# Performance work log

Measured on AMD Instinct MI355X. Metric: run time of the kernel, lower is better.

Reference implementation:

```python
import jax, jax.numpy as jnp
import numpy as np

DEPTH = 8
INPUT_DIM = 256
OUTPUT_DIM = 32
BATCH = 131072
N_INNER = 2 ** DEPTH - 1   # 255 inner nodes in heap/level order
N_LEAF = 2 ** DEPTH        # 256 leaves


def setup_inputs() -> dict:
    key = jax.random.key(0)
    kx, kw, kb, kbeta, kleaf = jax.random.split(key, 5)
    x = jax.random.normal(kx, (BATCH, INPUT_DIM), dtype=jnp.float32)
    # Stacked per-node Linear(input_dim, 1): weight rows [N_INNER, INPUT_DIM], bias [N_INNER]
    W = jax.random.normal(kw, (N_INNER, INPUT_DIM), dtype=jnp.float32) / np.sqrt(INPUT_DIM)
    b = jax.random.normal(kb, (N_INNER,), dtype=jnp.float32) * 0.01
    beta = jax.random.normal(kbeta, (N_INNER,), dtype=jnp.float32)  # per-node beta scalar
    leaf_param = jax.random.normal(kleaf, (N_LEAF, OUTPUT_DIM), dtype=jnp.float32)
    return {"x": x, "W": W, "b": b, "beta": beta, "leaf_param": leaf_param}


def _soft_tree(x, W, b, beta, leaf_param):
    B = x.shape[0]
    # All inner-node splits in one GEMM: sigmoid(beta_n * (x @ w_n + b_n))
    prob = jax.nn.sigmoid(beta[None, :] * (x @ W.T + b[None, :]))  # [B, N_INNER]
    # Level-wise path probability propagation (nodes stored in heap/level order).
    p = jnp.ones((B, 1), dtype=x.dtype)
    for d in range(DEPTH):
        lo = 2 ** d - 1
        pr = prob[:, lo: lo + 2 ** d]                      # [B, 2^d]
        # left child gets p*pr, right child gets p*(1-pr); interleave to keep DFS order
        p = jnp.stack([p * pr, p * (1.0 - pr)], axis=-1).reshape(B, 2 ** (d + 1))
    # leaf distributions Q = softmax(param) broadcast over batch; mixture output
    Q = jax.nn.softmax(leaf_param, axis=-1)                # [N_LEAF, OUTPUT_DIM]
    out = p @ Q                                            # [B, OUTPUT_DIM]
    return out, p


def reference(x, W, b, beta, leaf_param):
    out, path_probs = _soft_tree(x, W, b, beta, leaf_param)
    return out, path_probs
```

## Files before the change

### kernel.cpp

```cpp
#include <hip/hip_runtime.h>

#define BATCH   131072
#define IN_DIM  256
#define OUT_DIM 32
#define N_INNER 255
#define N_LEAF  256
#define OUT_HDR (BATCH * OUT_DIM)

#define TILE_M  64
#define BK      32
#define NTHR    512
#define NCHUNK  8
#define PSTR    260
#define INV64K  (1.0f / 65536.0f)

#define WS_QT_HI   0
#define WS_QT_LO   16384
#define WS_WIMG_HI 32768
#define WS_WIMG_LO (32768 + 131072)

#define WB0 0
#define WB1 32768
#define XB0 65536
#define XB1 73728
#define IMG_LO 34816
#define SMEM_BYTES 81920

typedef __attribute__((ext_vector_type(8))) short bf16x8;
typedef __attribute__((ext_vector_type(4))) float f32x4;

__device__ __forceinline__ unsigned short bf16rne(float a) {
    unsigned u = __float_as_uint(a);
    return (unsigned short)((u + 0x7FFFu + ((u >> 16) & 1u)) >> 16);
}
__device__ __forceinline__ unsigned packhi2(float a, float b) {
    return (unsigned)bf16rne(a) | ((unsigned)bf16rne(b) << 16);
}
__device__ __forceinline__ unsigned packlo2(float a, float b) {
    unsigned short ha = bf16rne(a), hb = bf16rne(b);
    float ra = a - __uint_as_float((unsigned)ha << 16);
    float rb = b - __uint_as_float((unsigned)hb << 16);
    return (unsigned)bf16rne(ra) | ((unsigned)bf16rne(rb) << 16);
}
__device__ __forceinline__ void split2(float a, float b, unsigned& hi, unsigned& lo) {
    unsigned short ha = bf16rne(a), hb = bf16rne(b);
    hi = (unsigned)ha | ((unsigned)hb << 16);
    float ra = a - __uint_as_float((unsigned)ha << 16);
    float rb = b - __uint_as_float((unsigned)hb << 16);
    lo = (unsigned)bf16rne(ra) | ((unsigned)bf16rne(rb) << 16);
}
__device__ __forceinline__ void tsplit2(float a, float b, unsigned& h, unsigned& l) {
    unsigned ua = __float_as_uint(a), ub = __float_as_uint(b);
    h = (ua >> 16) | (ub & 0xFFFF0000u);
    float ra = a - __uint_as_float(ua & 0xFFFF0000u);
    float rb = b - __uint_as_float(ub & 0xFFFF0000u);
    l = (__float_as_uint(ra) >> 16) | (__float_as_uint(rb) & 0xFFFF0000u);
}

__device__ __forceinline__ void gload16(const void* g, void* l) {
    __builtin_amdgcn_global_load_lds(
        (const __attribute__((address_space(1))) unsigned int*)g,
        (__attribute__((address_space(3))) unsigned int*)l, 16, 0, 0);
}

__global__ void wsplit_k(const float* __restrict__ W,
                         unsigned int* __restrict__ whi, unsigned int* __restrict__ wlo) {
    int gid = blockIdx.x * 512 + threadIdx.x;
    int n   = gid >> 5;
    int oct = gid & 31;
    float4 a = make_float4(0.f,0.f,0.f,0.f), b = a;
    if (n < N_INNER) {
        a = *(const float4*)(W + (size_t)n * IN_DIM + oct * 8);
        b = *(const float4*)(W + (size_t)n * IN_DIM + oct * 8 + 4);
    }
    uint4 h, l;
    split2(a.x, a.y, h.x, l.x); split2(a.z, a.w, h.y, l.y);
    split2(b.x, b.y, h.z, l.z); split2(b.z, b.w, h.w, l.w);
    int c = oct >> 2, kg = oct & 3;
    size_t off = ((size_t)(c * 4 + kg) * 256 + n) * 4;
    *(uint4*)(whi + off) = h;
    *(uint4*)(wlo + off) = l;
}

__global__ void qt_k(const float* __restrict__ leaf,
                     unsigned short* __restrict__ qhi, unsigned short* __restrict__ qlo) {
    int l = threadIdx.x;
    const float* row = leaf + l * OUT_DIM;
    float v[OUT_DIM];
    float mx = -1e30f;
#pragma unroll
    for (int o = 0; o < OUT_DIM; ++o) { v[o] = row[o]; mx = fmaxf(mx, v[o]); }
    float s = 0.f;
#pragma unroll
    for (int o = 0; o < OUT_DIM; ++o) { v[o] = __expf(v[o] - mx); s += v[o]; }
    float r = 1.f / s;
#pragma unroll
    for (int o = 0; o < OUT_DIM; ++o) {
        float q = v[o] * r;
        unsigned short h = bf16rne(q);
        float res = q - __uint_as_float((unsigned)h << 16);
        qhi[o * 256 + l] = h;
        qlo[o * 256 + l] = bf16rne(res);
    }
}

#define TREE_STAGE(D) { \
    const int base_ = (1 << (D)) - 1 + (qq << ((D) - 3)); \
    _Pragma("unroll") \
    for (int i = (1 << ((D) - 3)) - 1; i >= 0; --i) { \
        float pr_ = (float)pb[base_ + i] * INV64K; \
        float a_  = P[i]; \
        float lv_ = a_ * pr_; \
        P[2*i]     = lv_; \
        P[2*i + 1] = a_ - lv_; \
    } }

#define MFMA_BF16(A, B, C) __builtin_amdgcn_mfma_f32_16x16x32_bf16(A, B, C, 0, 0, 0)

__launch_bounds__(NTHR, 4)
__global__ void tree_k(const float* __restrict__ x,
                       const float* __restrict__ bv, const float* __restrict__ beta,
                       const unsigned short* __restrict__ qhi, const unsigned short* __restrict__ qlo,
                       const char* __restrict__ wimg_hi, const char* __restrict__ wimg_lo,
                       float* __restrict__ out) {
    extern __shared__ char smem[];
    const int tid  = threadIdx.x;
    const int row0 = blockIdx.x * TILE_M;

    const int lane  = tid & 63;
    const int w     = tid >> 6;
    const int col16 = lane & 15;
    const int hi4   = lane >> 4;
    const int wr    = w >> 2;
    const int wc    = w & 3;

    f32x4 acc[2][4];
#pragma unroll
    for (int i = 0; i < 2; ++i)
#pragma unroll
        for (int j = 0; j < 4; ++j) acc[i][j] = (f32x4){0.f, 0.f, 0.f, 0.f};

    const int xrow = tid >> 3;
    const int xkq  = tid & 7;
    const int xoff = (xkq >> 1) * 1024 + xrow * 16 + (xkq & 1) * 8;
    const float* xsrc = x + (size_t)(row0 + xrow) * IN_DIM + xkq * 4;

    {
        char* dh = smem + WB0 + w * 1024;
        char* dl = dh + 16384;
        gload16(wimg_hi + tid * 16,        dh);
        gload16(wimg_hi + 8192 + tid * 16, dh + 8192);
        gload16(wimg_lo + tid * 16,        dl);
        gload16(wimg_lo + 8192 + tid * 16, dl + 8192);
        float4 v = *(const float4*)(xsrc);
        uint2 h, l;
        tsplit2(v.x, v.y, h.x, l.x);
        tsplit2(v.z, v.w, h.y, l.y);
        *(uint2*)(smem + XB0 + xoff)        = h;
        *(uint2*)(smem + XB0 + 4096 + xoff) = l;
    }
    __syncthreads();

#pragma unroll 1
    for (int c = 0; c < NCHUNK; ++c) {
        const int cur = c & 1;
        const char* wb = smem + (cur ? WB1 : WB0);
        const char* xb = smem + (cur ? XB1 : XB0);
        char* wbn = smem + (cur ? WB0 : WB1);
        char* xbn = smem + (cur ? XB0 : XB1);

        float4 xn;
        const bool more = (c + 1 < NCHUNK);
        if (more) {
            const char* gh = wimg_hi + (size_t)(c + 1) * 16384;
            const char* gl = wimg_lo + (size_t)(c + 1) * 16384;
            char* dh = wbn + w * 1024;
            char* dl = dh + 16384;
            gload16(gh + tid * 16,        dh);
            gload16(gh + 8192 + tid * 16, dh + 8192);
            gload16(gl + tid * 16,        dl);
            gload16(gl + 8192 + tid * 16, dl + 8192);
            xn = *(const float4*)(xsrc + (c + 1) * BK);
        }

        bf16x8 ah[2], al[2];
#pragma unroll
        for (int rf = 0; rf < 2; ++rf) {
            int ao = hi4 * 1024 + (wr * 32 + rf * 16 + col16) * 16;
            ah[rf] = *(const bf16x8*)(xb + ao);
            al[rf] = *(const bf16x8*)(xb + 4096 + ao);
        }
#pragma unroll
        for (int cf = 0; cf < 4; ++cf) {
            int bo = hi4 * 4096 + (wc * 64 + cf * 16 + col16) * 16;
            bf16x8 bh = *(const bf16x8*)(wb + bo);
            bf16x8 bl = *(const bf16x8*)(wb + 16384 + bo);
#pragma unroll
            for (int rf = 0; rf < 2; ++rf) {
                acc[rf][cf] = MFMA_BF16(ah[rf], bh, acc[rf][cf]);
                acc[rf][cf] = MFMA_BF16(ah[rf], bl, acc[rf][cf]);
                acc[rf][cf] = MFMA_BF16(al[rf], bh, acc[rf][cf]);
            }
        }

        if (more) {
            uint2 h, l;
            tsplit2(xn.x, xn.y, h.x, l.x);
            tsplit2(xn.z, xn.w, h.y, l.y);
            *(uint2*)(xbn + xoff)        = h;
            *(uint2*)(xbn + 4096 + xoff) = l;
        }
        __syncthreads();
    }

    unsigned short* prob = (unsigned short*)smem;
    {
        float bb[4], bt[4];
#pragma unroll
        for (int cf = 0; cf < 4; ++cf) {
            int col = wc * 64 + cf * 16 + col16;
            bb[cf] = (col < N_INNER) ? bv[col]   : 0.f;
            bt[cf] = (col < N_INNER) ? beta[col] : 0.f;
        }
#pragma unroll
        for (int rf = 0; rf < 2; ++rf)
#pragma unroll
            for (int cf = 0; cf < 4; ++cf) {
                int col = wc * 64 + cf * 16 + col16;
#pragma unroll
                for (int r = 0; r < 4; ++r) {
                    int row = wr * 32 + rf * 16 + hi4 * 4 + r;
                    float t = (acc[rf][cf][r] + bb[cf]) * bt[cf];
                    float s = 1.f / (1.f + __expf(-t));
                    float u = fminf(s * 65536.f + 0.5f, 65535.f);
                    prob[row * PSTR + col] = (unsigned short)(unsigned)u;
                }
            }
    }
    __syncthreads();

    const int prow = tid >> 3;
    const int qq   = tid & 7;
    const unsigned short* pb = prob + prow * PSTR;
    float P[32];
    {
        float p0 = (float)pb[0] * INV64K;             float f0 = (qq & 4) ? (1.f - p0) : p0;
        float p1 = (float)pb[1 + (qq >> 2)] * INV64K; float f1 = (qq & 2) ? (1.f - p1) : p1;
        float p2 = (float)pb[3 + (qq >> 1)] * INV64K; float f2 = (qq & 1) ? (1.f - p2) : p2;
        P[0] = f0 * f1 * f2;
    }
    TREE_STAGE(3) TREE_STAGE(4) TREE_STAGE(5) TREE_STAGE(6) TREE_STAGE(7)

    {
        float* po = out + OUT_HDR + (size_t)(row0 + prow) * N_LEAF + qq * 32;
#pragma unroll
        for (int m = 0; m < 8; ++m)
            *(float4*)(po + m * 4) = make_float4(P[4*m], P[4*m+1], P[4*m+2], P[4*m+3]);
    }

#pragma unroll
    for (int kg = 0; kg < 4; ++kg) {
        uint4 l;
        l.x = packlo2(P[kg*8+0], P[kg*8+1]);
        l.y = packlo2(P[kg*8+2], P[kg*8+3]);
        l.z = packlo2(P[kg*8+4], P[kg*8+5]);
        l.w = packlo2(P[kg*8+6], P[kg*8+7]);
        *(uint4*)(smem + IMG_LO + qq * 4096 + kg * 1024 + ((prow * 16) ^ (qq << 4))) = l;
    }
    __syncthreads();

#pragma unroll
    for (int kg = 0; kg < 4; ++kg) {
        uint4 h;
        h.x = packhi2(P[kg*8+0], P[kg*8+1]);
        h.y = packhi2(P[kg*8+2], P[kg*8+3]);
        h.z = packhi2(P[kg*8+4], P[kg*8+5]);
        h.w = packhi2(P[kg*8+6], P[kg*8+7]);
        *(uint4*)(smem + qq * 4096 + kg * 1024 + ((prow * 16) ^ (qq << 4))) = h;
    }
    __syncthreads();

    f32x4 acc2 = (f32x4){0.f,0.f,0.f,0.f};
    const int cfw  = w >> 2;
    const int arow = (w & 3) * 16 + col16;
    const int qcol = (cfw * 16 + col16) * 256;

#pragma unroll
    for (int kc = 0; kc < 8; ++kc) {
        const int po = kc * 4096 + hi4 * 1024 + ((arow * 16) ^ (kc << 4));
        bf16x8 ph = *(const bf16x8*)(smem + po);
        bf16x8 pl = *(const bf16x8*)(smem + IMG_LO + po);
        int qo = qcol + kc * 32 + hi4 * 8;
        bf16x8 qbh = *(const bf16x8*)(qhi + qo);
        bf16x8 qbl = *(const bf16x8*)(qlo + qo);
        acc2 = MFMA_BF16(ph, qbh, acc2);
        acc2 = MFMA_BF16(ph, qbl, acc2);
        acc2 = MFMA_BF16(pl, qbh, acc2);
    }
#pragma unroll
    for (int r = 0; r < 4; ++r) {
        int row = (w & 3) * 16 + hi4 * 4 + r;
        out[(size_t)(row0 + row) * OUT_DIM + cfw * 16 + col16] = acc2[r];
    }
}

extern "C" void kernel_launch(void* const* d_in, const int* in_sizes, int n_in,
                              void* d_out, int out_size, void* d_ws, size_t ws_size,
                              hipStream_t stream) {
    const float* x    = (const float*)d_in[0];
    const float* W    = (const float*)d_in[1];
    const float* bv   = (const float*)d_in[2];
    const float* beta = (const float*)d_in[3];
    const float* leaf = (const float*)d_in[4];
    float* out = (float*)d_out;
    char* ws = (char*)d_ws;

    unsigned short* qhi = (unsigned short*)(ws + WS_QT_HI);
    unsigned short* qlo = (unsigned short*)(ws + WS_QT_LO);
    char* whi = ws + WS_WIMG_HI;
    char* wlo = ws + WS_WIMG_LO;

    hipFuncSetAttribute(reinterpret_cast<const void*>(tree_k),
                        hipFuncAttributeMaxDynamicSharedMemorySize, SMEM_BYTES);

    wsplit_k<<<16, 512, 0, stream>>>(W, (unsigned int*)whi, (unsigned int*)wlo);
    qt_k<<<1, 256, 0, stream>>>(leaf, qhi, qlo);
    tree_k<<<BATCH / TILE_M, NTHR, SMEM_BYTES, stream>>>(
        x, bv, beta, qhi, qlo, whi, wlo, out);
}
```

Baseline: 148.2 us.

## Shrink LDS footprint: stream W-lo from global, pad segments, reuse P image buffer

The W low-half bf16 image is no longer staged in LDS. Each wave reads its own W-lo fragments directly from global/L2 every chunk, which halves the weight double-buffer. W and x segments are padded (4128/1056-byte strides) to reduce LDS bank conflicts. The second GEMM now writes the P-hi and P-lo images one after the other into the same LDS region, separated by extra barriers. Together these cut shared memory per block so launch bounds can rise to 6 blocks/CU, trading extra global loads and syncs for higher occupancy.

```diff
diff --git a/kernel.cpp b/kernel.cpp
--- a/kernel.cpp
+++ b/kernel.cpp
@@ -19,12 +19,16 @@
 #define WS_WIMG_HI 32768
 #define WS_WIMG_LO (32768 + 131072)
 
-#define WB0 0
-#define WB1 32768
-#define XB0 65536
-#define XB1 73728
-#define IMG_LO 34816
-#define SMEM_BYTES 81920
+#define WSEG   4128
+#define WCH    (4 * WSEG)
+#define WB0    0
+#define WB1    WCH
+#define XSEG   1056
+#define XHALF  (4 * XSEG)
+#define XBUF   (2 * XHALF)
+#define XB0    (2 * WCH)
+#define XB1    (XB0 + XBUF)
+#define SMEM_BYTES (XB1 + XBUF)
 
 typedef __attribute__((ext_vector_type(8))) short bf16x8;
 typedef __attribute__((ext_vector_type(4))) float f32x4;
@@ -117,7 +121,7 @@
 
 #define MFMA_BF16(A, B, C) __builtin_amdgcn_mfma_f32_16x16x32_bf16(A, B, C, 0, 0, 0)
 
-__launch_bounds__(NTHR, 4)
+__launch_bounds__(NTHR, 6)
 __global__ void tree_k(const float* __restrict__ x,
                        const float* __restrict__ bv, const float* __restrict__ beta,
                        const unsigned short* __restrict__ qhi, const unsigned short* __restrict__ qlo,
@@ -142,22 +146,21 @@
 
     const int xrow = tid >> 3;
     const int xkq  = tid & 7;
-    const int xoff = (xkq >> 1) * 1024 + xrow * 16 + (xkq & 1) * 8;
+    const int xoff = (xkq >> 1) * XSEG + xrow * 16 + (xkq & 1) * 8;
     const float* xsrc = x + (size_t)(row0 + xrow) * IN_DIM + xkq * 4;
 
+    const int wdst = (w >> 2) * WSEG + (w & 3) * 1024;
+    const int lobase = hi4 * 4096 + (wc * 64 + col16) * 16;
+
     {
-        char* dh = smem + WB0 + w * 1024;
-        char* dl = dh + 16384;
-        gload16(wimg_hi + tid * 16,        dh);
-        gload16(wimg_hi + 8192 + tid * 16, dh + 8192);
-        gload16(wimg_lo + tid * 16,        dl);
-        gload16(wimg_lo + 8192 + tid * 16, dl + 8192);
+        gload16(wimg_hi + tid * 16,        smem + WB0 + wdst);
+        gload16(wimg_hi + 8192 + tid * 16, smem + WB0 + wdst + 2 * WSEG);
         float4 v = *(const float4*)(xsrc);
         uint2 h, l;
         tsplit2(v.x, v.y, h.x, l.x);
         tsplit2(v.z, v.w, h.y, l.y);
-        *(uint2*)(smem + XB0 + xoff)        = h;
-        *(uint2*)(smem + XB0 + 4096 + xoff) = l;
+        *(uint2*)(smem + XB0 + xoff)         = h;
+        *(uint2*)(smem + XB0 + XHALF + xoff) = l;
     }
     __syncthreads();
 
@@ -169,46 +172,49 @@
         char* wbn = smem + (cur ? WB0 : WB1);
         char* xbn = smem + (cur ? XB0 : XB1);
 
+        const char* blp = wimg_lo + (size_t)c * 16384 + lobase;
+        bf16x8 bl[4];
+#pragma unroll
+        for (int cf = 0; cf < 4; ++cf)
+            bl[cf] = *(const bf16x8*)(blp + cf * 256);
+
         float4 xn;
         const bool more = (c + 1 < NCHUNK);
         if (more) {
+            xn = *(const float4*)(xsrc + (c + 1) * BK);
             const char* gh = wimg_hi + (size_t)(c + 1) * 16384;
-            const char* gl = wimg_lo + (size_t)(c + 1) * 16384;
-            char* dh = wbn + w * 1024;
-            char* dl = dh + 16384;
-            gload16(gh + tid * 16,        dh);
-            gload16(gh + 8192 + tid * 16, dh + 8192);
-            gload16(gl + tid * 16,        dl);
-            gload16(gl + 8192 + tid * 16, dl + 8192);
-            xn = *(const float4*)(xsrc + (c + 1) * BK);
+            gload16(gh + tid * 16,        wbn + wdst);
+            gload16(gh + 8192 + tid * 16, wbn + wdst + 2 * WSEG);
         }
 
         bf16x8 ah[2], al[2];
 #pragma unroll
         for (int rf = 0; rf < 2; ++rf) {
-            int ao = hi4 * 1024 + (wr * 32 + rf * 16 + col16) * 16;
+            int ao = hi4 * XSEG + (wr * 32 + rf * 16 + col16) * 16;
             ah[rf] = *(const bf16x8*)(xb + ao);
-            al[rf] = *(const bf16x8*)(xb + 4096 + ao);
+            al[rf] = *(const bf16x8*)(xb + XHALF + ao);
         }
 #pragma unroll
         for (int cf = 0; cf < 4; ++cf) {
-            int bo = hi4 * 4096 + (wc * 64 + cf * 16 + col16) * 16;
+            int bo = hi4 * WSEG + (wc * 64 + cf * 16 + col16) * 16;
             bf16x8 bh = *(const bf16x8*)(wb + bo);
-            bf16x8 bl = *(const bf16x8*)(wb + 16384 + bo);
-#pragma unroll
-            for (int rf = 0; rf < 2; ++rf) {
-                acc[rf][cf] = MFMA_BF16(ah[rf], bh, acc[rf][cf]);
-                acc[rf][cf] = MFMA_BF16(ah[rf], bl, acc[rf][cf]);
-                acc[rf][cf] = MFMA_BF16(al[rf], bh, acc[rf][cf]);
-            }
+            acc[0][cf] = MFMA_BF16(ah[0], bh, acc[0][cf]);
+            acc[1][cf] = MFMA_BF16(ah[1], bh, acc[1][cf]);
+            acc[0][cf] = MFMA_BF16(al[0], bh, acc[0][cf]);
+            acc[1][cf] = MFMA_BF16(al[1], bh, acc[1][cf]);
+        }
+#pragma unroll
+        for (int cf = 0; cf < 4; ++cf) {
+            acc[0][cf] = MFMA_BF16(ah[0], bl[cf], acc[0][cf]);
+            acc[1][cf] = MFMA_BF16(ah[1], bl[cf], acc[1][cf]);
         }
 
         if (more) {
             uint2 h, l;
             tsplit2(xn.x, xn.y, h.x, l.x);
             tsplit2(xn.z, xn.w, h.y, l.y);
-            *(uint2*)(xbn + xoff)        = h;
-            *(uint2*)(xbn + 4096 + xoff) = l;
+            *(uint2*)(xbn + xoff)         = h;
+            *(uint2*)(xbn + XHALF + xoff) = l;
         }
         __syncthreads();
     }
@@ -257,16 +263,6 @@
         for (int m = 0; m < 8; ++m)
             *(float4*)(po + m * 4) = make_float4(P[4*m], P[4*m+1], P[4*m+2], P[4*m+3]);
     }
-
-#pragma unroll
-    for (int kg = 0; kg < 4; ++kg) {
-        uint4 l;
-        l.x = packlo2(P[kg*8+0], P[kg*8+1]);
-        l.y = packlo2(P[kg*8+2], P[kg*8+3]);
-        l.z = packlo2(P[kg*8+4], P[kg*8+5]);
-        l.w = packlo2(P[kg*8+6], P[kg*8+7]);
-        *(uint4*)(smem + IMG_LO + qq * 4096 + kg * 1024 + ((prow * 16) ^ (qq << 4))) = l;
-    }
     __syncthreads();
 
 #pragma unroll
@@ -287,15 +283,32 @@
 
 #pragma unroll
     for (int kc = 0; kc < 8; ++kc) {
-        const int po = kc * 4096 + hi4 * 1024 + ((arow * 16) ^ (kc << 4));
-        bf16x8 ph = *(const bf16x8*)(smem + po);
-        bf16x8 pl = *(const bf16x8*)(smem + IMG_LO + po);
+        bf16x8 pa = *(const bf16x8*)(smem + kc * 4096 + hi4 * 1024 + ((arow * 16) ^ (kc << 4)));
         int qo = qcol + kc * 32 + hi4 * 8;
         bf16x8 qbh = *(const bf16x8*)(qhi + qo);
         bf16x8 qbl = *(const bf16x8*)(qlo + qo);
-        acc2 = MFMA_BF16(ph, qbh, acc2);
-        acc2 = MFMA_BF16(ph, qbl, acc2);
-        acc2 = MFMA_BF16(pl, qbh, acc2);
+        acc2 = MFMA_BF16(pa, qbh, acc2);
+        acc2 = MFMA_BF16(pa, qbl, acc2);
+    }
+    __syncthreads();
+
+#pragma unroll
+    for (int kg = 0; kg < 4; ++kg) {
+        uint4 l;
+        l.x = packlo2(P[kg*8+0], P[kg*8+1]);
+        l.y = packlo2(P[kg*8+2], P[kg*8+3]);
+        l.z = packlo2(P[kg*8+4], P[kg*8+5]);
+        l.w = packlo2(P[kg*8+6], P[kg*8+7]);
+        *(uint4*)(smem + qq * 4096 + kg * 1024 + ((prow * 16) ^ (qq << 4))) = l;
+    }
+    __syncthreads();
+
+#pragma unroll
+    for (int kc = 0; kc < 8; ++kc) {
+        bf16x8 pa = *(const bf16x8*)(smem + kc * 4096 + hi4 * 1024 + ((arow * 16) ^ (kc << 4)));
+        int qo = qcol + kc * 32 + hi4 * 8;
+        bf16x8 qbh = *(const bf16x8*)(qhi + qo);
+        acc2 = MFMA_BF16(pa, qbh, acc2);
     }
 #pragma unroll
     for (int r = 0; r < 4; ++r) {
```

Result: slower. 184.2 us (+24.3%).

## Prefetch x two chunks ahead and relax barrier waits to vmcnt(1)

Applied to the files above, without the earlier changes.

Loads of x from global memory are now issued two K-chunks ahead and held in registers, so the newest x load can stay in flight across the barrier. The barriers use an explicit s_waitcnt vmcnt(1) instead of a full __syncthreads drain. To keep the wait count uniform, the last iterations issue redundant loads of the final W chunk and x chunk. The aim is to hide global load latency behind the MFMA work, at the cost of extra redundant traffic and a fragile dependence on the order of the vmcnt counter.

```diff
diff --git a/kernel.cpp b/kernel.cpp
--- a/kernel.cpp
+++ b/kernel.cpp
@@ -145,21 +145,26 @@
     const int xoff = (xkq >> 1) * 1024 + xrow * 16 + (xkq & 1) * 8;
     const float* xsrc = x + (size_t)(row0 + xrow) * IN_DIM + xkq * 4;
 
+    float4 xv;
     {
+        float4 x0 = *(const float4*)(xsrc);
         char* dh = smem + WB0 + w * 1024;
         char* dl = dh + 16384;
         gload16(wimg_hi + tid * 16,        dh);
         gload16(wimg_hi + 8192 + tid * 16, dh + 8192);
         gload16(wimg_lo + tid * 16,        dl);
         gload16(wimg_lo + 8192 + tid * 16, dl + 8192);
-        float4 v = *(const float4*)(xsrc);
+        xv = *(const float4*)(xsrc + BK);
         uint2 h, l;
-        tsplit2(v.x, v.y, h.x, l.x);
-        tsplit2(v.z, v.w, h.y, l.y);
+        tsplit2(x0.x, x0.y, h.x, l.x);
+        tsplit2(x0.z, x0.w, h.y, l.y);
         *(uint2*)(smem + XB0 + xoff)        = h;
         *(uint2*)(smem + XB0 + 4096 + xoff) = l;
     }
-    __syncthreads();
+    asm volatile("s_waitcnt vmcnt(1) lgkmcnt(0)" ::: "memory");
+    __builtin_amdgcn_sched_barrier(0);
+    __builtin_amdgcn_s_barrier();
+    __builtin_amdgcn_sched_barrier(0);
 
 #pragma unroll 1
     for (int c = 0; c < NCHUNK; ++c) {
@@ -169,19 +174,19 @@
         char* wbn = smem + (cur ? WB0 : WB1);
         char* xbn = smem + (cur ? XB0 : XB1);
 
-        float4 xn;
-        const bool more = (c + 1 < NCHUNK);
-        if (more) {
-            const char* gh = wimg_hi + (size_t)(c + 1) * 16384;
-            const char* gl = wimg_lo + (size_t)(c + 1) * 16384;
+        {
+            const int cn = (c + 1 < NCHUNK) ? c + 1 : NCHUNK - 1;
+            const char* gh = wimg_hi + (size_t)cn * 16384;
+            const char* gl = wimg_lo + (size_t)cn * 16384;
             char* dh = wbn + w * 1024;
             char* dl = dh + 16384;
             gload16(gh + tid * 16,        dh);
             gload16(gh + 8192 + tid * 16, dh + 8192);
             gload16(gl + tid * 16,        dl);
             gload16(gl + 8192 + tid * 16, dl + 8192);
-            xn = *(const float4*)(xsrc + (c + 1) * BK);
-        }
+        }
+        const int cn2 = (c + 2 < NCHUNK) ? c + 2 : NCHUNK - 1;
+        float4 xn = *(const float4*)(xsrc + cn2 * BK);
 
         bf16x8 ah[2], al[2];
 #pragma unroll
@@ -203,15 +208,24 @@
             }
         }
 
-        if (more) {
+        {
             uint2 h, l;
-            tsplit2(xn.x, xn.y, h.x, l.x);
-            tsplit2(xn.z, xn.w, h.y, l.y);
+            tsplit2(xv.x, xv.y, h.x, l.x);
+            tsplit2(xv.z, xv.w, h.y, l.y);
             *(uint2*)(xbn + xoff)        = h;
             *(uint2*)(xbn + 4096 + xoff) = l;
         }
-        __syncthreads();
-    }
+        xv = xn;
+
+        asm volatile("s_waitcnt vmcnt(1) lgkmcnt(0)" ::: "memory");
+        __builtin_amdgcn_sched_barrier(0);
+        __builtin_amdgcn_s_barrier();
+        __builtin_amdgcn_sched_barrier(0);
+    }
+
+    asm volatile("s_waitcnt vmcnt(0) lgkmcnt(0)" ::: "memory");
+    __builtin_amdgcn_sched_barrier(0);
+    __builtin_amdgcn_s_barrier();
 
     unsigned short* prob = (unsigned short*)smem;
     {
```

After: 151.8 us. 2.4% more time.

## Double row tile to 128, single-buffer W, restructure tree and leaf GEMM

Applied to the files above, without the earlier changes.

Doubles the rows per block to 128 so each W chunk loaded into shared memory serves twice as many rows, halving total W traffic and the number of blocks. W becomes single-buffered: barriers with explicit waitcnt now separate the MFMA reads from the next chunk's loads, while x stays double-buffered with a padded layout. The tree propagation now gives each thread 64 leaves instead of 32. The leaf mixture GEMM is reorganized so each wave computes both 16-column output tiles, with the hi and lo P images staged in shared memory one after the other. The cost is more accumulator registers (16 f32x4 tiles) and likely lower occupancy, and the W load is no longer overlapped with compute.

```diff
diff --git a/kernel.cpp b/kernel.cpp
--- a/kernel.cpp
+++ b/kernel.cpp
@@ -7,11 +7,11 @@
 #define N_LEAF  256
 #define OUT_HDR (BATCH * OUT_DIM)
 
-#define TILE_M  64
+#define TILE_M  128
 #define BK      32
 #define NTHR    512
 #define NCHUNK  8
-#define PSTR    260
+#define PSTR    272
 #define INV64K  (1.0f / 65536.0f)
 
 #define WS_QT_HI   0
@@ -19,12 +19,13 @@
 #define WS_WIMG_HI 32768
 #define WS_WIMG_LO (32768 + 131072)
 
-#define WB0 0
-#define WB1 32768
-#define XB0 65536
-#define XB1 73728
-#define IMG_LO 34816
-#define SMEM_BYTES 81920
+#define WBUF 0
+#define XSEG 2080
+#define XHALF 8320
+#define XBSZ  16640
+#define XB0   32768
+#define XB1   49408
+#define SMEM_BYTES 69632
 
 typedef __attribute__((ext_vector_type(8))) short bf16x8;
 typedef __attribute__((ext_vector_type(4))) float f32x4;
@@ -105,9 +106,9 @@
 }
 
 #define TREE_STAGE(D) { \
-    const int base_ = (1 << (D)) - 1 + (qq << ((D) - 3)); \
+    const int base_ = (1 << (D)) - 1 + (qq << ((D) - 2)); \
     _Pragma("unroll") \
-    for (int i = (1 << ((D) - 3)) - 1; i >= 0; --i) { \
+    for (int i = (1 << ((D) - 2)) - 1; i >= 0; --i) { \
         float pr_ = (float)pb[base_ + i] * INV64K; \
         float a_  = P[i]; \
         float lv_ = a_ * pr_; \
@@ -134,83 +135,91 @@
     const int wr    = w >> 2;
     const int wc    = w & 3;
 
-    f32x4 acc[2][4];
-#pragma unroll
-    for (int i = 0; i < 2; ++i)
+    f32x4 acc[4][4];
+#pragma unroll
+    for (int i = 0; i < 4; ++i)
 #pragma unroll
         for (int j = 0; j < 4; ++j) acc[i][j] = (f32x4){0.f, 0.f, 0.f, 0.f};
 
-    const int xrow = tid >> 3;
-    const int xkq  = tid & 7;
-    const int xoff = (xkq >> 1) * 1024 + xrow * 16 + (xkq & 1) * 8;
-    const float* xsrc = x + (size_t)(row0 + xrow) * IN_DIM + xkq * 4;
+    const int xrow = tid >> 2;
+    const int xk   = tid & 3;
+    const int xwoff = xk * XSEG + xrow * 16;
+    const float* xsrc = x + (size_t)(row0 + xrow) * IN_DIM + xk * 8;
 
     {
-        char* dh = smem + WB0 + w * 1024;
+        char* dh = smem + WBUF + w * 1024;
         char* dl = dh + 16384;
         gload16(wimg_hi + tid * 16,        dh);
         gload16(wimg_hi + 8192 + tid * 16, dh + 8192);
         gload16(wimg_lo + tid * 16,        dl);
         gload16(wimg_lo + 8192 + tid * 16, dl + 8192);
-        float4 v = *(const float4*)(xsrc);
-        uint2 h, l;
-        tsplit2(v.x, v.y, h.x, l.x);
-        tsplit2(v.z, v.w, h.y, l.y);
-        *(uint2*)(smem + XB0 + xoff)        = h;
-        *(uint2*)(smem + XB0 + 4096 + xoff) = l;
-    }
-    __syncthreads();
+        float4 a = *(const float4*)(xsrc);
+        float4 b = *(const float4*)(xsrc + 4);
+        uint4 h, l;
+        tsplit2(a.x, a.y, h.x, l.x); tsplit2(a.z, a.w, h.y, l.y);
+        tsplit2(b.x, b.y, h.z, l.z); tsplit2(b.z, b.w, h.w, l.w);
+        *(uint4*)(smem + XB0 + xwoff)         = h;
+        *(uint4*)(smem + XB0 + XHALF + xwoff) = l;
+    }
+    asm volatile("s_waitcnt vmcnt(0) lgkmcnt(0)" ::: "memory");
+    __builtin_amdgcn_sched_barrier(0);
+    __builtin_amdgcn_s_barrier();
+    __builtin_amdgcn_sched_barrier(0);
 
 #pragma unroll 1
     for (int c = 0; c < NCHUNK; ++c) {
-        const int cur = c & 1;
-        const char* wb = smem + (cur ? WB1 : WB0);
-        const char* xb = smem + (cur ? XB1 : XB0);
-        char* wbn = smem + (cur ? WB0 : WB1);
-        char* xbn = smem + (cur ? XB0 : XB1);
-
-        float4 xn;
+        const char* xb  = smem + ((c & 1) ? XB1 : XB0);
+        char*       xbn = smem + ((c & 1) ? XB0 : XB1);
         const bool more = (c + 1 < NCHUNK);
+
+        bf16x8 ah[4], al[4];
+#pragma unroll
+        for (int rf = 0; rf < 4; ++rf) {
+            int ao = hi4 * XSEG + (wr * 64 + rf * 16 + col16) * 16;
+            ah[rf] = *(const bf16x8*)(xb + ao);
+            al[rf] = *(const bf16x8*)(xb + XHALF + ao);
+        }
+#pragma unroll
+        for (int cf = 0; cf < 4; ++cf) {
+            int bo = hi4 * 4096 + (wc * 64 + cf * 16 + col16) * 16;
+            bf16x8 bh = *(const bf16x8*)(smem + WBUF + bo);
+            bf16x8 bl = *(const bf16x8*)(smem + WBUF + 16384 + bo);
+#pragma unroll
+            for (int rf = 0; rf < 4; ++rf) {
+                acc[rf][cf] = MFMA_BF16(ah[rf], bh, acc[rf][cf]);
+                acc[rf][cf] = MFMA_BF16(al[rf], bh, acc[rf][cf]);
+                acc[rf][cf] = MFMA_BF16(ah[rf], bl, acc[rf][cf]);
+            }
+        }
+
+        if (more) {
+            float4 a = *(const float4*)(xsrc + (c + 1) * BK);
+            float4 b = *(const float4*)(xsrc + (c + 1) * BK + 4);
+            uint4 h, l;
+            tsplit2(a.x, a.y, h.x, l.x); tsplit2(a.z, a.w, h.y, l.y);
+            tsplit2(b.x, b.y, h.z, l.z); tsplit2(b.z, b.w, h.w, l.w);
+            *(uint4*)(xbn + xwoff)         = h;
+            *(uint4*)(xbn + XHALF + xwoff) = l;
+        }
+        asm volatile("s_waitcnt lgkmcnt(0)" ::: "memory");
+        __builtin_amdgcn_sched_barrier(0);
+        __builtin_amdgcn_s_barrier();
+        __builtin_amdgcn_sched_barrier(0);
+
         if (more) {
             const char* gh = wimg_hi + (size_t)(c + 1) * 16384;
             const char* gl = wimg_lo + (size_t)(c + 1) * 16384;
-            char* dh = wbn + w * 1024;
+            char* dh = smem + WBUF + w * 1024;
             char* dl = dh + 16384;
             gload16(gh + tid * 16,        dh);
             gload16(gh + 8192 + tid * 16, dh + 8192);
             gload16(gl + tid * 16,        dl);
             gload16(gl + 8192 + tid * 16, dl + 8192);
-            xn = *(const float4*)(xsrc + (c + 1) * BK);
-        }
-
-        bf16x8 ah[2], al[2];
-#pragma unroll
-        for (int rf = 0; rf < 2; ++rf) {
-            int ao = hi4 * 1024 + (wr * 32 + rf * 16 + col16) * 16;
-            ah[rf] = *(const bf16x8*)(xb + ao);
-            al[rf] = *(const bf16x8*)(xb + 4096 + ao);
-        }
-#pragma unroll
-        for (int cf = 0; cf < 4; ++cf) {
-            int bo = hi4 * 4096 + (wc * 64 + cf * 16 + col16) * 16;
-            bf16x8 bh = *(const bf16x8*)(wb + bo);
-            bf16x8 bl = *(const bf16x8*)(wb + 16384 + bo);
-#pragma unroll
-            for (int rf = 0; rf < 2; ++rf) {
-                acc[rf][cf] = MFMA_BF16(ah[rf], bh, acc[rf][cf]);
-                acc[rf][cf] = MFMA_BF16(ah[rf], bl, acc[rf][cf]);
-                acc[rf][cf] = MFMA_BF16(al[rf], bh, acc[rf][cf]);
-            }
-        }
-
-        if (more) {
-            uint2 h, l;
-            tsplit2(xn.x, xn.y, h.x, l.x);
-            tsplit2(xn.z, xn.w, h.y, l.y);
-            *(uint2*)(xbn + xoff)        = h;
-            *(uint2*)(xbn + 4096 + xoff) = l;
-        }
-        __syncthreads();
+            asm volatile("s_waitcnt vmcnt(0)" ::: "memory");
+            __builtin_amdgcn_sched_barrier(0);
+            __builtin_amdgcn_s_barrier();
+            __builtin_amdgcn_sched_barrier(0);
+        }
     }
 
     unsigned short* prob = (unsigned short*)smem;
@@ -223,13 +232,13 @@
             bt[cf] = (col < N_INNER) ? beta[col] : 0.f;
         }
 #pragma unroll
-        for (int rf = 0; rf < 2; ++rf)
+        for (int rf = 0; rf < 4; ++rf)
 #pragma unroll
             for (int cf = 0; cf < 4; ++cf) {
                 int col = wc * 64 + cf * 16 + col16;
 #pragma unroll
                 for (int r = 0; r < 4; ++r) {
-                    int row = wr * 32 + rf * 16 + hi4 * 4 + r;
+                    int row = wr * 64 + rf * 16 + hi4 * 4 + r;
                     float t = (acc[rf][cf][r] + bb[cf]) * bt[cf];
                     float s = 1.f / (1.f + __expf(-t));
                     float u = fminf(s * 65536.f + 0.5f, 65535.f);
@@ -239,69 +248,89 @@
     }
     __syncthreads();
 
-    const int prow = tid >> 3;
-    const int qq   = tid & 7;
+    const int prow = tid >> 2;
+    const int qq   = tid & 3;
     const unsigned short* pb = prob + prow * PSTR;
-    float P[32];
+    float P[64];
     {
-        float p0 = (float)pb[0] * INV64K;             float f0 = (qq & 4) ? (1.f - p0) : p0;
-        float p1 = (float)pb[1 + (qq >> 2)] * INV64K; float f1 = (qq & 2) ? (1.f - p1) : p1;
-        float p2 = (float)pb[3 + (qq >> 1)] * INV64K; float f2 = (qq & 1) ? (1.f - p2) : p2;
-        P[0] = f0 * f1 * f2;
-    }
-    TREE_STAGE(3) TREE_STAGE(4) TREE_STAGE(5) TREE_STAGE(6) TREE_STAGE(7)
+        float p0 = (float)pb[0] * INV64K;             float f0 = (qq & 2) ? (1.f - p0) : p0;
+        float p1 = (float)pb[1 + (qq >> 1)] * INV64K; float f1 = (qq & 1) ? (1.f - p1) : p1;
+        P[0] = f0 * f1;
+    }
+    TREE_STAGE(2) TREE_STAGE(3) TREE_STAGE(4) TREE_STAGE(5) TREE_STAGE(6) TREE_STAGE(7)
 
     {
-        float* po = out + OUT_HDR + (size_t)(row0 + prow) * N_LEAF + qq * 32;
-#pragma unroll
-        for (int m = 0; m < 8; ++m)
+        float* po = out + OUT_HDR + (size_t)(row0 + prow) * N_LEAF + qq * 64;
+#pragma unroll
+        for (int m = 0; m < 16; ++m)
             *(float4*)(po + m * 4) = make_float4(P[4*m], P[4*m+1], P[4*m+2], P[4*m+3]);
     }
-
-#pragma unroll
-    for (int kg = 0; kg < 4; ++kg) {
-        uint4 l;
-        l.x = packlo2(P[kg*8+0], P[kg*8+1]);
-        l.y = packlo2(P[kg*8+2], P[kg*8+3]);
-        l.z = packlo2(P[kg*8+4], P[kg*8+5]);
-        l.w = packlo2(P[kg*8+6], P[kg*8+7]);
-        *(uint4*)(smem + IMG_LO + qq * 4096 + kg * 1024 + ((prow * 16) ^ (qq << 4))) = l;
-    }
-    __syncthreads();
-
-#pragma unroll
-    for (int kg = 0; kg < 4; ++kg) {
-        uint4 h;
-        h.x = packhi2(P[kg*8+0], P[kg*8+1]);
-        h.y = packhi2(P[kg*8+2], P[kg*8+3]);
-        h.z = packhi2(P[kg*8+4], P[kg*8+5]);
-        h.w = packhi2(P[kg*8+6], P[kg*8+7]);
-        *(uint4*)(smem + qq * 4096 + kg * 1024 + ((prow * 16) ^ (qq << 4))) = h;
-    }
-    __syncthreads();
-
-    f32x4 acc2 = (f32x4){0.f,0.f,0.f,0.f};
-    const int cfw  = w >> 2;
-    const int arow = (w & 3) * 16 + col16;
-    const int qcol = (cfw * 16 + col16) * 256;
+    __syncthreads();
+
+#pragma unroll
+    for (int kk = 0; kk < 2; ++kk)
+#pragma unroll
+        for (int g = 0; g < 4; ++g) {
+            int b = kk * 32 + g * 8;
+            uint4 h;
+            h.x = packhi2(P[b+0], P[b+1]);
+            h.y = packhi2(P[b+2], P[b+3]);
+            h.z = packhi2(P[b+4], P[b+5]);
+            h.w = packhi2(P[b+6], P[b+7]);
+            *(uint4*)(smem + (2*qq + kk) * 8192 + g * 2048 + prow * 16 + qq * 32) = h;
+        }
+    __syncthreads();
+
+    f32x4 acc2[2];
+    acc2[0] = (f32x4){0.f,0.f,0.f,0.f};
+    acc2[1] = (f32x4){0.f,0.f,0.f,0.f};
+    const int arow = w * 16 + col16;
 
 #pragma unroll
     for (int kc = 0; kc < 8; ++kc) {
-        const int po = kc * 4096 + hi4 * 1024 + ((arow * 16) ^ (kc << 4));
-        bf16x8 ph = *(const bf16x8*)(smem + po);
-        bf16x8 pl = *(const bf16x8*)(smem + IMG_LO + po);
-        int qo = qcol + kc * 32 + hi4 * 8;
-        bf16x8 qbh = *(const bf16x8*)(qhi + qo);
-        bf16x8 qbl = *(const bf16x8*)(qlo + qo);
-        acc2 = MFMA_BF16(ph, qbh, acc2);
-        acc2 = MFMA_BF16(ph, qbl, acc2);
-        acc2 = MFMA_BF16(pl, qbh, acc2);
-    }
-#pragma unroll
-    for (int r = 0; r < 4; ++r) {
-        int row = (w & 3) * 16 + hi4 * 4 + r;
-        out[(size_t)(row0 + row) * OUT_DIM + cfw * 16 + col16] = acc2[r];
-    }
+        bf16x8 pa = *(const bf16x8*)(smem + kc * 8192 + hi4 * 2048 + arow * 16 + (kc >> 1) * 32);
+#pragma unroll
+        for (int cf = 0; cf < 2; ++cf) {
+            int qo = (cf * 16 + col16) * 256 + kc * 32 + hi4 * 8;
+            bf16x8 qbh = *(const bf16x8*)(qhi + qo);
+            bf16x8 qbl = *(const bf16x8*)(qlo + qo);
+            acc2[cf] = MFMA_BF16(pa, qbh, acc2[cf]);
+            acc2[cf] = MFMA_BF16(pa, qbl, acc2[cf]);
+        }
+    }
+    __syncthreads();
+
+#pragma unroll
+    for (int kk = 0; kk < 2; ++kk)
+#pragma unroll
+        for (int g = 0; g < 4; ++g) {
+            int b = kk * 32 + g * 8;
+            uint4 l;
+            l.x = packlo2(P[b+0], P[b+1]);
+            l.y = packlo2(P[b+2], P[b+3]);
+            l.z = packlo2(P[b+4], P[b+5]);
+            l.w = packlo2(P[b+6], P[b+7]);
+            *(uint4*)(smem + (2*qq + kk) * 8192 + g * 2048 + prow * 16 + qq * 32) = l;
+        }
+    __syncthreads();
+
+#pragma unroll
+    for (int kc = 0; kc < 8; ++kc) {
+        bf16x8 pl = *(const bf16x8*)(smem + kc * 8192 + hi4 * 2048 + arow * 16 + (kc >> 1) * 32);
+#pragma unroll
+        for (int cf = 0; cf < 2; ++cf) {
+            int qo = (cf * 16 + col16) * 256 + kc * 32 + hi4 * 8;
+            bf16x8 qbh = *(const bf16x8*)(qhi + qo);
+            acc2[cf] = MFMA_BF16(pl, qbh, acc2[cf]);
+        }
+    }
+#pragma unroll
+    for (int cf = 0; cf < 2; ++cf)
+#pragma unroll
+        for (int r = 0; r < 4; ++r) {
+            int row = w * 16 + hi4 * 4 + r;
+            out[(size_t)(row0 + row) * OUT_DIM + cf * 16 + col16] = acc2[cf][r];
+        }
 }
 
 extern "C" void kernel_launch(void* const* d_in, const int* in_sizes, int n_in,
```

Result: no change. 147.9 us, median of 2 (-0.2%).
